# Optimization experiments

Measured on AMD Instinct MI355X. Metric: run time of the kernel, lower is better.

The kernel has to match this reference:

```python
import jax, jax.numpy as jnp
import numpy as np

HEADS = 8


def setup_inputs() -> dict:
    key = jax.random.key(0)
    ks = jax.random.split(key, 5)
    B, C, H, W = 2, 256, 48, 48
    s = 0.02
    return {
        "ct": jax.random.normal(ks[0], (B, C, H, W), jnp.float32),
        "us": jax.random.normal(ks[1], (B, C, H, W), jnp.float32),
        "w_qkv_ct": jax.random.normal(ks[2], (3 * C, C), jnp.float32) * s,
        "w_qkv_us": jax.random.normal(ks[3], (3 * C, C), jnp.float32) * s,
        "w_proj": jax.random.normal(ks[4], (C, 2 * C), jnp.float32) * s,
        "b_proj": jnp.zeros((C,), jnp.float32),
    }


def _heads_view(x, B, H, W):
    # [B, C, H, W] -> [B, heads, HW, dh]
    C = x.shape[1]
    return x.reshape(B, HEADS, C // HEADS, H * W).transpose(0, 1, 3, 2)


def _cross_attn(q, k, v, scale):
    # q,k,v: [B, heads, HW, dh]
    attn = jax.nn.softmax(jnp.einsum("bhnd,bhmd->bhnm", q, k) * scale, axis=-1)
    return jnp.einsum("bhnm,bhmd->bhnd", attn, v)


def reference(ct, us, w_qkv_ct, w_qkv_us, w_proj, b_proj):
    B, C, H, W = ct.shape
    dh = C // HEADS
    scale = dh ** (-0.5)

    # 1x1 convs as channel GEMMs
    qkv1 = jnp.einsum("oc,bchw->bohw", w_qkv_ct, ct)
    qkv2 = jnp.einsum("oc,bchw->bohw", w_qkv_us, us)
    q1, k1, v1 = jnp.split(qkv1, 3, axis=1)
    q2, k2, v2 = jnp.split(qkv2, 3, axis=1)

    # CT queries attend to US keys/values
    o1 = _cross_attn(_heads_view(q1, B, H, W), _heads_view(k2, B, H, W),
                     _heads_view(v2, B, H, W), scale)
    # US queries attend to CT keys/values
    o2 = _cross_attn(_heads_view(q2, B, H, W), _heads_view(k1, B, H, W),
                     _heads_view(v1, B, H, W), scale)

    # [B, heads, HW, dh] -> [B, C, H, W]
    out1 = o1.transpose(0, 1, 3, 2).reshape(B, C, H, W)
    out2 = o2.transpose(0, 1, 3, 2).reshape(B, C, H, W)

    fused = jnp.concatenate([ct + out1, us + out2], axis=1)
    return jnp.einsum("oc,bchw->bohw", w_proj, fused) + b_proj[None, :, None, None]
```

## Files before the change

### kernel.cpp

```cpp
#include <hip/hip_runtime.h>
#include <hip/hip_bf16.h>
#include <math.h>

#define HW   2304
#define CCH  256

#define QSCALE 0.25504368686637270f

typedef short short8 __attribute__((ext_vector_type(8)));
typedef float f32x4  __attribute__((ext_vector_type(4)));

__device__ inline unsigned short f2bf(float f) {
    union { float f; unsigned u; } v; v.f = f;
    unsigned r = v.u + 0x7FFF + ((v.u >> 16) & 1);
    return (unsigned short)(r >> 16);
}
__device__ inline float bf2f(unsigned short u) {
    union { unsigned u; float f; } v; v.u = ((unsigned)u) << 16;
    return v.f;
}
__device__ inline unsigned pkbf2(float a, float b) {
    float2 f; f.x = a; f.y = b;
    union { __hip_bfloat162 h; unsigned u; } c;
    c.h = __float22bfloat162_rn(f);
    return c.u;
}
__device__ inline unsigned pktrunc(float a, float b) {
    return __builtin_amdgcn_perm(__builtin_bit_cast(unsigned, b),
                                 __builtin_bit_cast(unsigned, a), 0x07060302u);
}

__global__ __launch_bounds__(256, 4) void prep_k(
    const float* __restrict__ ct, const float* __restrict__ us,
    const float* __restrict__ w1, const float* __restrict__ w2,
    const float* __restrict__ w3,
    unsigned short* __restrict__ xT,
    unsigned short* __restrict__ b1, unsigned short* __restrict__ b2,
    unsigned short* __restrict__ b3)
{
    const int bx = blockIdx.x, t = threadIdx.x;
    if (bx >= 576) {
        const int v_ = bx - 576;
        int z, base;
        if (v_ < 192)      { z = 0; base = v_ * 1024; }
        else if (v_ < 384) { z = 1; base = (v_ - 192) * 1024; }
        else               { z = 2; base = (v_ - 384) * 1024; }
        const float* s = (z == 0) ? w1 : (z == 1) ? w2 : w3;
        unsigned short* d = (z == 0) ? b1 : (z == 1) ? b2 : b3;
        const int i = base + t * 4;
        const float4 v4 = *(const float4*)&s[i];
        const float sc = (z < 2 && i < 65536) ? QSCALE : 1.f;
        uint2 p; p.x = pkbf2(v4.x * sc, v4.y * sc); p.y = pkbf2(v4.z * sc, v4.w * sc);
        *(uint2*)&d[i] = p;
        return;
    }
    const int pt = bx % 36, rest = bx / 36, ctile = rest & 3, z = rest >> 2;
    const float* __restrict__ src = ((z >> 1) ? us : ct) + (size_t)(z & 1) * CCH * HW;
    unsigned short* __restrict__ dst = xT + (size_t)z * HW * 256;
    const int p0 = pt * 64, c0 = ctile * 64;
    __shared__ __align__(16) unsigned short Ts[64 * 72];
#pragma unroll
    for (int r = 0; r < 4; r++) {
        const int c = (t >> 4) + 16 * r;
        const float4 v4 = *(const float4*)&src[(size_t)(c0 + c) * HW + p0 + (t & 15) * 4];
        Ts[((t & 15) * 4 + 0) * 72 + c] = f2bf(v4.x);
        Ts[((t & 15) * 4 + 1) * 72 + c] = f2bf(v4.y);
        Ts[((t & 15) * 4 + 2) * 72 + c] = f2bf(v4.z);
        Ts[((t & 15) * 4 + 3) * 72 + c] = f2bf(v4.w);
    }
    __syncthreads();
    const int p = t >> 2, c8 = (t & 3) * 16;
    const short8 a  = *(const short8*)&Ts[p * 72 + c8];
    const short8 b8 = *(const short8*)&Ts[p * 72 + c8 + 8];
    *(short8*)&dst[(size_t)(p0 + p) * 256 + c0 + c8]     = a;
    *(short8*)&dst[(size_t)(p0 + p) * 256 + c0 + c8 + 8] = b8;
}

__global__ __launch_bounds__(256, 4) void qkv_k(
    const unsigned short* __restrict__ xT,
    const unsigned short* __restrict__ wb1, const unsigned short* __restrict__ wb2,
    unsigned short* __restrict__ qkvT1, unsigned short* __restrict__ qkvT2,
    unsigned short* __restrict__ vdm1,  unsigned short* __restrict__ vdm2)
{
    const int inp = blockIdx.z >> 1, b = blockIdx.z & 1;
    const unsigned short* __restrict__ X = xT + (size_t)(inp * 2 + b) * HW * 256;
    const unsigned short* __restrict__ W = inp ? wb2 : wb1;
    unsigned short* __restrict__ qT = (inp ? qkvT2 : qkvT1) + (size_t)b * HW * 512;
    unsigned short* __restrict__ vd = (inp ? vdm2 : vdm1) + (size_t)b * CCH * HW;
    const int p0 = blockIdx.x * 64, o0 = blockIdx.y * 64;
    __shared__ __align__(16) unsigned short Ws[64 * 72];
    __shared__ __align__(16) unsigned short Xs[64 * 72];
    const int t = threadIdx.x, w = t >> 6, lane = t & 63, quad = lane >> 4, m = lane & 15;
    const int sr = t >> 3, sc = t & 7;

    f32x4 acc[4] = {{0,0,0,0},{0,0,0,0},{0,0,0,0},{0,0,0,0}};
    for (int k0 = 0; k0 < 256; k0 += 64) {
        const short8 wv0 = *(const short8*)&W[(size_t)(o0 + sr) * 256 + k0 + sc * 8];
        const short8 wv1 = *(const short8*)&W[(size_t)(o0 + 32 + sr) * 256 + k0 + sc * 8];
        const short8 xv0 = *(const short8*)&X[(size_t)(p0 + sr) * 256 + k0 + sc * 8];
        const short8 xv1 = *(const short8*)&X[(size_t)(p0 + 32 + sr) * 256 + k0 + sc * 8];
        __syncthreads();
        *(short8*)&Ws[sr * 72 + sc * 8] = wv0;
        *(short8*)&Ws[(32 + sr) * 72 + sc * 8] = wv1;
        *(short8*)&Xs[sr * 72 + sc * 8] = xv0;
        *(short8*)&Xs[(32 + sr) * 72 + sc * 8] = xv1;
        __syncthreads();
#pragma unroll
        for (int kc2 = 0; kc2 < 2; kc2++) {
            const short8 af = *(const short8*)&Ws[(w * 16 + m) * 72 + kc2 * 32 + quad * 8];
#pragma unroll
            for (int pg = 0; pg < 4; pg++) {
                const short8 bf = *(const short8*)&Xs[(pg * 16 + m) * 72 + kc2 * 32 + quad * 8];
                acc[pg] = __builtin_amdgcn_mfma_f32_16x16x32_bf16(af, bf, acc[pg], 0, 0, 0);
            }
        }
    }
    __syncthreads();
    if (o0 < 512) {
#pragma unroll
        for (int pg = 0; pg < 4; pg++) {
            uint2 pk; pk.x = pkbf2(acc[pg][0], acc[pg][1]); pk.y = pkbf2(acc[pg][2], acc[pg][3]);
            *(uint2*)&Ws[(pg * 16 + m) * 72 + w * 16 + quad * 4] = pk;
        }
        __syncthreads();
        const int pr = t >> 2, cc = t & 3;
        const uint4 d0 = *(const uint4*)&Ws[pr * 72 + cc * 16];
        const uint4 d1 = *(const uint4*)&Ws[pr * 72 + cc * 16 + 8];
        *(uint4*)&qT[(size_t)(p0 + pr) * 512 + o0 + cc * 16]     = d0;
        *(uint4*)&qT[(size_t)(p0 + pr) * 512 + o0 + cc * 16 + 8] = d1;
    } else {
#pragma unroll
        for (int pg = 0; pg < 4; pg++)
#pragma unroll
            for (int r = 0; r < 4; r++)
                Ws[(w * 16 + quad * 4 + r) * 72 + pg * 16 + m] = f2bf(acc[pg][r]);
        __syncthreads();
        const int dr = t >> 2, cc = t & 3;
        const uint4 d0 = *(const uint4*)&Ws[dr * 72 + cc * 16];
        const uint4 d1 = *(const uint4*)&Ws[dr * 72 + cc * 16 + 8];
        *(uint4*)&vd[(size_t)(o0 - 512 + dr) * HW + p0 + cc * 16]     = d0;
        *(uint4*)&vd[(size_t)(o0 - 512 + dr) * HW + p0 + cc * 16 + 8] = d1;
    }
}

__global__ __launch_bounds__(256, 4) void attn_k(
    const unsigned short* __restrict__ qkvT1, const unsigned short* __restrict__ qkvT2,
    const unsigned short* __restrict__ vdm1,  const unsigned short* __restrict__ vdm2,
    unsigned short* __restrict__ pOb, float* __restrict__ pL)
{
    const int dir = blockIdx.z >> 1, s = blockIdx.z & 1;
    const int b = blockIdx.y >> 3, h = blockIdx.y & 7;
    const int inst = (dir * 2 + b) * 8 + h;
    const unsigned short* __restrict__ Qt = (dir ? qkvT2 : qkvT1) + (size_t)b * HW * 512;
    const unsigned short* __restrict__ Kt = (dir ? qkvT1 : qkvT2) + (size_t)b * HW * 512
                                            + 256 + h * 32;
    const unsigned short* __restrict__ Vd = (dir ? vdm1 : vdm2) + ((size_t)b * CCH + h * 32) * HW;

    const int t = threadIdx.x, w = t >> 6, lane = t & 63, quad = lane >> 4, m = lane & 15;

    __shared__ __align__(16) unsigned short Ks[128 * 32];
    __shared__ __align__(16) unsigned short Vs[32 * 136];

    const int pq0 = blockIdx.x * 128 + w * 32 + m;
    const int pq1 = pq0 + 16;
    const short8 qf0 = *(const short8*)&Qt[(size_t)pq0 * 512 + h * 32 + quad * 8];
    const short8 qf1 = *(const short8*)&Qt[(size_t)pq1 * 512 + h * 32 + quad * 8];

    f32x4 acc00 = {0,0,0,0}, acc10 = {0,0,0,0};
    f32x4 acc01 = {0,0,0,0}, acc11 = {0,0,0,0};
    f32x4 accl0 = {0,0,0,0}, accl1 = {0,0,0,0};
    const short ONE = (short)0x3F80;
    const short8 ones = {ONE,ONE,ONE,ONE,ONE,ONE,ONE,ONE};

    const int kj0 = t >> 2, kcs = t & 3;
    const int pcK = kcs ^ (((kj0 >> 1) & 1) | (((kj0 >> 3) & 1) << 1));
    const int vr0 = t >> 4, vcs = t & 15;
    const int g2m = ((m >> 1) & 1) | (((m >> 2) & 1) << 1);
    const unsigned short* __restrict__ ksb =
        &Ks[((m >> 2) * 8 + (m & 3)) * 32 + (quad ^ g2m) * 8];
    const unsigned short* __restrict__ vsb = &Vs[m * 136 + quad * 8];

    const int jlo = s * 1152, jhi = jlo + 1152;
    short8 ka = *(const short8*)&Kt[(size_t)(jlo + kj0) * 512 + kcs * 8];
    short8 kb = *(const short8*)&Kt[(size_t)(jlo + kj0 + 64) * 512 + kcs * 8];
    short8 va = *(const short8*)&Vd[(size_t)vr0 * HW + jlo + vcs * 8];
    short8 vb = *(const short8*)&Vd[(size_t)(vr0 + 16) * HW + jlo + vcs * 8];

    for (int j0 = jlo; j0 < jhi; j0 += 128) {
        __syncthreads();
        *(short8*)&Ks[kj0 * 32 + pcK * 8] = ka;
        *(short8*)&Ks[(kj0 + 64) * 32 + pcK * 8] = kb;
        *(short8*)&Vs[vr0 * 136 + vcs * 8] = va;
        *(short8*)&Vs[(vr0 + 16) * 136 + vcs * 8] = vb;
        const int jn = (j0 + 128 < jhi) ? j0 + 128 : jlo;
        ka = *(const short8*)&Kt[(size_t)(jn + kj0) * 512 + kcs * 8];
        kb = *(const short8*)&Kt[(size_t)(jn + kj0 + 64) * 512 + kcs * 8];
        va = *(const short8*)&Vd[(size_t)vr0 * HW + jn + vcs * 8];
        vb = *(const short8*)&Vd[(size_t)(vr0 + 16) * HW + jn + vcs * 8];
        __syncthreads();

        uint4 pw4a[4], pw4b[4];
#pragma unroll
        for (int f = 0; f < 8; f++) {
            const short8 kf = *(const short8*)(ksb + ((f >> 1) * 32 + (f & 1) * 4) * 32);
            const f32x4 z = {0,0,0,0};
            const f32x4 S0 = __builtin_amdgcn_mfma_f32_16x16x32_bf16(kf, qf0, z, 0, 0, 0);
            const f32x4 S1 = __builtin_amdgcn_mfma_f32_16x16x32_bf16(kf, qf1, z, 0, 0, 0);
            const unsigned pa0 = pktrunc(__builtin_amdgcn_exp2f(S0[0]), __builtin_amdgcn_exp2f(S0[1]));
            const unsigned pa1 = pktrunc(__builtin_amdgcn_exp2f(S0[2]), __builtin_amdgcn_exp2f(S0[3]));
            const unsigned pb0 = pktrunc(__builtin_amdgcn_exp2f(S1[0]), __builtin_amdgcn_exp2f(S1[1]));
            const unsigned pb1 = pktrunc(__builtin_amdgcn_exp2f(S1[2]), __builtin_amdgcn_exp2f(S1[3]));
            if ((f & 1) == 0) {
                pw4a[f >> 1].x = pa0; pw4a[f >> 1].y = pa1;
                pw4b[f >> 1].x = pb0; pw4b[f >> 1].y = pb1;
            } else {
                pw4a[f >> 1].z = pa0; pw4a[f >> 1].w = pa1;
                pw4b[f >> 1].z = pb0; pw4b[f >> 1].w = pb1;
            }
        }
#pragma unroll
        for (int kt = 0; kt < 4; kt++) {
            const short8 pf0 = __builtin_bit_cast(short8, pw4a[kt]);
            const short8 pf1 = __builtin_bit_cast(short8, pw4b[kt]);
            const short8 vf0 = *(const short8*)(vsb + kt * 32);
            const short8 vf1 = *(const short8*)(vsb + 16 * 136 + kt * 32);
            acc00 = __builtin_amdgcn_mfma_f32_16x16x32_bf16(vf0, pf0, acc00, 0, 0, 0);
            acc10 = __builtin_amdgcn_mfma_f32_16x16x32_bf16(vf1, pf0, acc10, 0, 0, 0);
            acc01 = __builtin_amdgcn_mfma_f32_16x16x32_bf16(vf0, pf1, acc01, 0, 0, 0);
            acc11 = __builtin_amdgcn_mfma_f32_16x16x32_bf16(vf1, pf1, acc11, 0, 0, 0);
            accl0 = __builtin_amdgcn_mfma_f32_16x16x32_bf16(ones, pf0, accl0, 0, 0, 0);
            accl1 = __builtin_amdgcn_mfma_f32_16x16x32_bf16(ones, pf1, accl1, 0, 0, 0);
        }
    }

    unsigned short* __restrict__ po = pOb + (size_t)(inst * 2 + s) * 32 * HW;
    float* __restrict__ pl = pL + (size_t)(inst * 2 + s) * HW;
#pragma unroll
    for (int qi = 0; qi < 2; qi++) {
        const int pq = qi ? pq1 : pq0;
        const f32x4 aL = qi ? acc01 : acc00;
        const f32x4 aH = qi ? acc11 : acc10;
#pragma unroll
        for (int r = 0; r < 4; r++) {
            po[(size_t)(quad * 4 + r) * HW + pq]      = f2bf(aL[r]);
            po[(size_t)(16 + quad * 4 + r) * HW + pq] = f2bf(aH[r]);
        }
        if (quad == 0) pl[pq] = qi ? accl1[0] : accl0[0];
    }
}

__global__ __launch_bounds__(256, 8) void merge_k(
    const unsigned short* __restrict__ pOb, const float* __restrict__ pL,
    const float* __restrict__ ct, const float* __restrict__ us,
    unsigned short* __restrict__ fusedT)
{
    const int inst = blockIdx.y;
    const int dir = inst >> 4, b = (inst >> 3) & 1, h = inst & 7;
    const unsigned short* __restrict__ p0 = pOb + (size_t)(inst * 2 + 0) * 32 * HW;
    const unsigned short* __restrict__ p1 = pOb + (size_t)(inst * 2 + 1) * 32 * HW;
    const float* __restrict__ src = (dir ? us : ct) + ((size_t)b * CCH + h * 32) * HW;
    const int t = threadIdx.x, q = blockIdx.x * 64 + (t & 63), dg = (t >> 6) * 8;

    const float inv = 1.f / (pL[(size_t)(inst * 2 + 0) * HW + q] +
                             pL[(size_t)(inst * 2 + 1) * HW + q]);
    float v[8];
#pragma unroll
    for (int i = 0; i < 8; i++) {
        const int d = dg + i;
        v[i] = (bf2f(p0[(size_t)d * HW + q]) + bf2f(p1[(size_t)d * HW + q])) * inv
               + src[(size_t)d * HW + q];
    }
    uint4 pk;
    pk.x = pkbf2(v[0], v[1]); pk.y = pkbf2(v[2], v[3]);
    pk.z = pkbf2(v[4], v[5]); pk.w = pkbf2(v[6], v[7]);
    *(uint4*)&fusedT[((size_t)b * HW + q) * 512 + dir * 256 + h * 32 + dg] = pk;
}

__global__ __launch_bounds__(256, 4) void proj_k(
    const unsigned short* __restrict__ w3b, const unsigned short* __restrict__ fusedT,
    const float* __restrict__ bias, float* __restrict__ out)
{
    const int p0 = blockIdx.x * 64, o0 = blockIdx.y * 64;
    __shared__ __align__(16) unsigned short Ws[64 * 72];
    __shared__ __align__(16) unsigned short Xs[64 * 72];
    const int t = threadIdx.x, w = t >> 6, lane = t & 63, quad = lane >> 4, m = lane & 15;
    const int sr = t >> 3, sc = t & 7;

    f32x4 acc[4] = {{0,0,0,0},{0,0,0,0},{0,0,0,0},{0,0,0,0}};
    for (int k0 = 0; k0 < 512; k0 += 64) {
        const short8 wv0 = *(const short8*)&w3b[(size_t)(o0 + sr) * 512 + k0 + sc * 8];
        const short8 wv1 = *(const short8*)&w3b[(size_t)(o0 + 32 + sr) * 512 + k0 + sc * 8];
        const short8 xv0 = *(const short8*)&fusedT[(size_t)(p0 + sr) * 512 + k0 + sc * 8];
        const short8 xv1 = *(const short8*)&fusedT[(size_t)(p0 + 32 + sr) * 512 + k0 + sc * 8];
        __syncthreads();
        *(short8*)&Ws[sr * 72 + sc * 8] = wv0;
        *(short8*)&Ws[(32 + sr) * 72 + sc * 8] = wv1;
        *(short8*)&Xs[sr * 72 + sc * 8] = xv0;
        *(short8*)&Xs[(32 + sr) * 72 + sc * 8] = xv1;
        __syncthreads();
#pragma unroll
        for (int kc2 = 0; kc2 < 2; kc2++) {
            const short8 af = *(const short8*)&Ws[(w * 16 + m) * 72 + kc2 * 32 + quad * 8];
#pragma unroll
            for (int pg = 0; pg < 4; pg++) {
                const short8 bf = *(const short8*)&Xs[(pg * 16 + m) * 72 + kc2 * 32 + quad * 8];
                acc[pg] = __builtin_amdgcn_mfma_f32_16x16x32_bf16(af, bf, acc[pg], 0, 0, 0);
            }
        }
    }
    const int b = (p0 >= HW) ? 1 : 0;
    const int pl0 = p0 - b * HW;
    float* __restrict__ ob = out + (size_t)b * CCH * HW;
    float b4[4];
#pragma unroll
    for (int r = 0; r < 4; r++) b4[r] = bias[o0 + w * 16 + quad * 4 + r];
#pragma unroll
    for (int pg = 0; pg < 4; pg++)
#pragma unroll
        for (int r = 0; r < 4; r++)
            ob[(size_t)(o0 + w * 16 + quad * 4 + r) * HW + pl0 + pg * 16 + m]
                = acc[pg][r] + b4[r];
}

extern "C" void kernel_launch(void* const* d_in, const int* in_sizes, int n_in,
                              void* d_out, int out_size, void* d_ws, size_t ws_size,
                              hipStream_t stream)
{
    const float* ct       = (const float*)d_in[0];
    const float* us       = (const float*)d_in[1];
    const float* w_qkv_ct = (const float*)d_in[2];
    const float* w_qkv_us = (const float*)d_in[3];
    const float* w_proj   = (const float*)d_in[4];
    const float* b_proj   = (const float*)d_in[5];
    float* out = (float*)d_out;

    unsigned short* wb1   = (unsigned short*)d_ws;
    unsigned short* wb2   = wb1 + (size_t)768 * 256;
    unsigned short* w3b   = wb2 + (size_t)768 * 256;
    unsigned short* xT    = w3b + (size_t)256 * 512;
    unsigned short* qkvT1 = xT    + (size_t)4 * HW * 256;
    unsigned short* qkvT2 = qkvT1 + (size_t)2 * HW * 512;
    unsigned short* vdm1  = qkvT2 + (size_t)2 * HW * 512;
    unsigned short* vdm2  = vdm1  + (size_t)2 * CCH * HW;
    unsigned short* fusedT= vdm2  + (size_t)2 * CCH * HW;
    unsigned short* pOb   = fusedT + (size_t)2 * HW * 512;
    float*          pL    = (float*)(pOb + (size_t)64 * 32 * HW);

    prep_k <<<dim3(1088), 256, 0, stream>>>(ct, us, w_qkv_ct, w_qkv_us, w_proj,
                                            xT, wb1, wb2, w3b);
    qkv_k  <<<dim3(36, 12, 4), 256, 0, stream>>>(xT, wb1, wb2, qkvT1, qkvT2, vdm1, vdm2);
    attn_k <<<dim3(18, 16, 4), 256, 0, stream>>>(qkvT1, qkvT2, vdm1, vdm2, pOb, pL);
    merge_k<<<dim3(36, 32), 256, 0, stream>>>(pOb, pL, ct, us, fusedT);
    proj_k <<<dim3(72, 4), 256, 0, stream>>>(w3b, fusedT, b_proj, out);
}
```

Before: 128.3 us.

## Halve attention query tile per block and raise occupancy hint

The attention kernel now processes 64 queries per block (16 per wave) instead of 128, with the grid doubled and launch bounds raised to 8 blocks per CU. This cuts per-thread accumulators and registers so more waves can be resident to hide latency. The cost is that each staged K/V tile is reused by half as many queries, doubling K/V load and LDS staging work per unit of compute.

```diff
diff --git a/kernel.cpp b/kernel.cpp
--- a/kernel.cpp
+++ b/kernel.cpp
@@ -143,7 +143,7 @@
     }
 }
 
-__global__ __launch_bounds__(256, 4) void attn_k(
+__global__ __launch_bounds__(256, 8) void attn_k(
     const unsigned short* __restrict__ qkvT1, const unsigned short* __restrict__ qkvT2,
     const unsigned short* __restrict__ vdm1,  const unsigned short* __restrict__ vdm2,
     unsigned short* __restrict__ pOb, float* __restrict__ pL)
@@ -161,14 +161,10 @@
     __shared__ __align__(16) unsigned short Ks[128 * 32];
     __shared__ __align__(16) unsigned short Vs[32 * 136];
 
-    const int pq0 = blockIdx.x * 128 + w * 32 + m;
-    const int pq1 = pq0 + 16;
-    const short8 qf0 = *(const short8*)&Qt[(size_t)pq0 * 512 + h * 32 + quad * 8];
-    const short8 qf1 = *(const short8*)&Qt[(size_t)pq1 * 512 + h * 32 + quad * 8];
-
-    f32x4 acc00 = {0,0,0,0}, acc10 = {0,0,0,0};
-    f32x4 acc01 = {0,0,0,0}, acc11 = {0,0,0,0};
-    f32x4 accl0 = {0,0,0,0}, accl1 = {0,0,0,0};
+    const int pq = blockIdx.x * 64 + w * 16 + m;
+    const short8 qf = *(const short8*)&Qt[(size_t)pq * 512 + h * 32 + quad * 8];
+
+    f32x4 acc0 = {0,0,0,0}, acc1 = {0,0,0,0}, accl = {0,0,0,0};
     const short ONE = (short)0x3F80;
     const short8 ones = {ONE,ONE,ONE,ONE,ONE,ONE,ONE,ONE};
 
@@ -199,54 +195,38 @@
         vb = *(const short8*)&Vd[(size_t)(vr0 + 16) * HW + jn + vcs * 8];
         __syncthreads();
 
-        uint4 pw4a[4], pw4b[4];
+        uint4 pw4[4];
 #pragma unroll
         for (int f = 0; f < 8; f++) {
             const short8 kf = *(const short8*)(ksb + ((f >> 1) * 32 + (f & 1) * 4) * 32);
             const f32x4 z = {0,0,0,0};
-            const f32x4 S0 = __builtin_amdgcn_mfma_f32_16x16x32_bf16(kf, qf0, z, 0, 0, 0);
-            const f32x4 S1 = __builtin_amdgcn_mfma_f32_16x16x32_bf16(kf, qf1, z, 0, 0, 0);
-            const unsigned pa0 = pktrunc(__builtin_amdgcn_exp2f(S0[0]), __builtin_amdgcn_exp2f(S0[1]));
-            const unsigned pa1 = pktrunc(__builtin_amdgcn_exp2f(S0[2]), __builtin_amdgcn_exp2f(S0[3]));
-            const unsigned pb0 = pktrunc(__builtin_amdgcn_exp2f(S1[0]), __builtin_amdgcn_exp2f(S1[1]));
-            const unsigned pb1 = pktrunc(__builtin_amdgcn_exp2f(S1[2]), __builtin_amdgcn_exp2f(S1[3]));
-            if ((f & 1) == 0) {
-                pw4a[f >> 1].x = pa0; pw4a[f >> 1].y = pa1;
-                pw4b[f >> 1].x = pb0; pw4b[f >> 1].y = pb1;
-            } else {
-                pw4a[f >> 1].z = pa0; pw4a[f >> 1].w = pa1;
-                pw4b[f >> 1].z = pb0; pw4b[f >> 1].w = pb1;
-            }
+            const f32x4 S = __builtin_amdgcn_mfma_f32_16x16x32_bf16(kf, qf, z, 0, 0, 0);
+            const float e0 = __builtin_amdgcn_exp2f(S[0]);
+            const float e1 = __builtin_amdgcn_exp2f(S[1]);
+            const float e2 = __builtin_amdgcn_exp2f(S[2]);
+            const float e3 = __builtin_amdgcn_exp2f(S[3]);
+            if ((f & 1) == 0) { pw4[f >> 1].x = pktrunc(e0, e1); pw4[f >> 1].y = pktrunc(e2, e3); }
+            else              { pw4[f >> 1].z = pktrunc(e0, e1); pw4[f >> 1].w = pktrunc(e2, e3); }
         }
 #pragma unroll
         for (int kt = 0; kt < 4; kt++) {
-            const short8 pf0 = __builtin_bit_cast(short8, pw4a[kt]);
-            const short8 pf1 = __builtin_bit_cast(short8, pw4b[kt]);
+            const short8 pf = __builtin_bit_cast(short8, pw4[kt]);
             const short8 vf0 = *(const short8*)(vsb + kt * 32);
             const short8 vf1 = *(const short8*)(vsb + 16 * 136 + kt * 32);
-            acc00 = __builtin_amdgcn_mfma_f32_16x16x32_bf16(vf0, pf0, acc00, 0, 0, 0);
-            acc10 = __builtin_amdgcn_mfma_f32_16x16x32_bf16(vf1, pf0, acc10, 0, 0, 0);
-            acc01 = __builtin_amdgcn_mfma_f32_16x16x32_bf16(vf0, pf1, acc01, 0, 0, 0);
-            acc11 = __builtin_amdgcn_mfma_f32_16x16x32_bf16(vf1, pf1, acc11, 0, 0, 0);
-            accl0 = __builtin_amdgcn_mfma_f32_16x16x32_bf16(ones, pf0, accl0, 0, 0, 0);
-            accl1 = __builtin_amdgcn_mfma_f32_16x16x32_bf16(ones, pf1, accl1, 0, 0, 0);
+            acc0 = __builtin_amdgcn_mfma_f32_16x16x32_bf16(vf0, pf, acc0, 0, 0, 0);
+            acc1 = __builtin_amdgcn_mfma_f32_16x16x32_bf16(vf1, pf, acc1, 0, 0, 0);
+            accl = __builtin_amdgcn_mfma_f32_16x16x32_bf16(ones, pf, accl, 0, 0, 0);
         }
     }
 
     unsigned short* __restrict__ po = pOb + (size_t)(inst * 2 + s) * 32 * HW;
     float* __restrict__ pl = pL + (size_t)(inst * 2 + s) * HW;
 #pragma unroll
-    for (int qi = 0; qi < 2; qi++) {
-        const int pq = qi ? pq1 : pq0;
-        const f32x4 aL = qi ? acc01 : acc00;
-        const f32x4 aH = qi ? acc11 : acc10;
-#pragma unroll
-        for (int r = 0; r < 4; r++) {
-            po[(size_t)(quad * 4 + r) * HW + pq]      = f2bf(aL[r]);
-            po[(size_t)(16 + quad * 4 + r) * HW + pq] = f2bf(aH[r]);
-        }
-        if (quad == 0) pl[pq] = qi ? accl1[0] : accl0[0];
-    }
+    for (int r = 0; r < 4; r++) {
+        po[(size_t)(quad * 4 + r) * HW + pq]      = f2bf(acc0[r]);
+        po[(size_t)(16 + quad * 4 + r) * HW + pq] = f2bf(acc1[r]);
+    }
+    if (quad == 0) pl[pq] = accl[0];
 }
 
 __global__ __launch_bounds__(256, 8) void merge_k(
@@ -349,7 +329,7 @@
     prep_k <<<dim3(1088), 256, 0, stream>>>(ct, us, w_qkv_ct, w_qkv_us, w_proj,
                                             xT, wb1, wb2, w3b);
     qkv_k  <<<dim3(36, 12, 4), 256, 0, stream>>>(xT, wb1, wb2, qkvT1, qkvT2, vdm1, vdm2);
-    attn_k <<<dim3(18, 16, 4), 256, 0, stream>>>(qkvT1, qkvT2, vdm1, vdm2, pOb, pL);
+    attn_k <<<dim3(36, 16, 4), 256, 0, stream>>>(qkvT1, qkvT2, vdm1, vdm2, pOb, pL);
     merge_k<<<dim3(36, 32), 256, 0, stream>>>(pOb, pL, ct, us, fusedT);
     proj_k <<<dim3(72, 4), 256, 0, stream>>>(w3b, fusedT, b_proj, out);
 }
```

New measurement: 129.4 us. Within noise of the previous version (+0.9%).
